# Kernel optimization log

Hardware: AMD Instinct MI355X
Metric: run time of the kernel (lower is better)

The kernel has to match this reference:

```python
import jax, jax.numpy as jnp
import numpy as np

# --- sizes / simulation constants (match init_kwargs) ---
IN_F, OUT_F, BIAS = 512, 512, 1
BATCH = 128
RES, SIM_TIME, TAU_SYN = 1e-4, 2e-2, 5e-3
STEPS = int(np.ceil(SIM_TIME / RES))                 # 200
DECAY_SYN = float(np.exp(-RES / TAU_SYN))
DECAY_MEM = float(np.exp(-RES / TAU_SYN))            # original code uses tau_syn for both


def setup_inputs() -> dict:
    key = jax.random.key(0)
    k1, k2, k3, k4 = jax.random.split(key, 4)
    # input spikes inside the first half of the sim window
    input_times = jax.random.uniform(k1, (BATCH, IN_F), jnp.float32) * (0.5 * SIM_TIME)
    # weights_init = (0.05, 0.1) normal
    weights = 0.05 + 0.1 * jax.random.normal(k2, (IN_F + BIAS, OUT_F), jnp.float32)
    # delays_init = (0.001, 0.0005) normal, kept non-negative
    delays = jnp.abs(0.001 + 0.0005 * jax.random.normal(k3, (IN_F + BIAS, OUT_F), jnp.float32))
    # thresholds_init = (1.0, 0.05) normal
    thresholds = 1.0 + 0.05 * jax.random.normal(k4, (OUT_F,), jnp.float32)
    return {"input_times": input_times, "weights": weights,
            "delays": delays, "thresholds": thresholds}


def _snn_forward(input_times, weights, delays, thresholds):
    B = input_times.shape[0]
    dt = input_times.dtype
    # bias inputs spike at t = 0
    times = jnp.concatenate([input_times, jnp.zeros((B, BIAS), dt)], axis=1)   # [B, I+bias]
    # per-synapse delayed arrival times -> time-step indices
    arrival = times[:, :, None] + delays[None]                                  # [B, I+bias, O]
    step_idx = jnp.clip(jnp.round(arrival / RES).astype(jnp.int32), 0, STEPS - 1)
    b_idx = jnp.arange(B)[:, None, None]
    o_idx = jnp.arange(OUT_F)[None, None, :]
    w = jnp.broadcast_to(weights[None], arrival.shape)
    # charge[b, t, o] = sum_i w[i,o] * 1[arrival step of synapse (i,o) == t]
    charge = jnp.zeros((B, STEPS, OUT_F), dt).at[b_idx, step_idx, o_idx].add(w)
    charge = jnp.moveaxis(charge, 1, 0)                                         # [steps, B, O]

    thr = thresholds[None]                                                      # [1, O]

    def body(carry, inp):
        syn, mem, spike_t, spiked = carry
        t, c = inp
        syn_n = syn * DECAY_SYN + c
        mem_n = mem * DECAY_MEM + (1.0 - DECAY_MEM) * syn_n
        crossing = jnp.logical_and(~spiked, mem_n >= thr)
        denom = mem_n - mem
        safe = jnp.where(jnp.abs(denom) > 1e-12, denom, 1e-12)
        frac = jnp.clip((thr - mem) / safe, 0.0, 1.0)     # linear interp inside the step
        t_cross = (t + frac) * RES
        spike_t = jnp.where(crossing, t_cross, spike_t)
        spiked = jnp.logical_or(spiked, crossing)
        return (syn_n, mem_n, spike_t, spiked), None

    init = (jnp.zeros((B, OUT_F), dt),
            jnp.zeros((B, OUT_F), dt),
            jnp.full((B, OUT_F), SIM_TIME, dt),           # "no spike" -> sim_time
            jnp.zeros((B, OUT_F), bool))
    ts = jnp.arange(STEPS, dtype=dt)
    (syn, mem, spike_t, spiked), _ = jax.lax.scan(body, init, (ts, charge))
    return spike_t                                        # [B, O] first-spike times


def reference(input_times, weights, delays, thresholds):
    return _snn_forward(input_times, weights, delays, thresholds)
```

## Files before the change

### kernel.cpp

```cpp
#include <hip/hip_runtime.h>


#define IN_F    512
#define OUT_F   512
#define BATCH   128
#define STEPS   200
#define RES_F   1e-4f
#define CSTRIDE 33
#define DECAY_F 0.98019867330675525f
#define ONEMD_F 0.019801326693244747f
#define SIM_T_F 2e-2f
#define FPSCALE 8388608.0f
#define INVSCALE 1.1920928955078125e-07f

__device__ __forceinline__ int bin_of(float arr) {
    float q = (float)((double)arr * 10000.0);
    int s = __float2int_rn(q);
    return s > STEPS - 1 ? STEPS - 1 : s;
}

__global__ __launch_bounds__(512, 4) void snn_fwd(
    const float* __restrict__ input_times,
    const float* __restrict__ weights,
    const float* __restrict__ delays,
    const float* __restrict__ thresholds,
    float* __restrict__ out)
{
#pragma clang fp contract(off)
    __shared__ __align__(16) int chargeI[2][STEPS * CSTRIDE];
    __shared__ float times_s[2][IN_F];

    const int tid  = threadIdx.x;
    const int wv   = tid >> 6;
    const int lane = tid & 63;
    const int b0    = (blockIdx.x >> 4) << 1;
    const int otile = blockIdx.x & 15;
    const int ob    = otile << 5;

    {
        int4 z = make_int4(0, 0, 0, 0);
        int4* c4 = (int4*)&chargeI[0][0];
        for (int k = tid; k < (2 * STEPS * CSTRIDE) / 4; k += 512) c4[k] = z;
    }
    times_s[0][tid] = input_times[b0 * IN_F + tid];
    times_s[1][tid] = input_times[(b0 + 1) * IN_F + tid];
    __syncthreads();

    const int sub = lane >> 3;
    const int cgi = lane & 7;
    const int cg  = cgi << 2;
    const float4* __restrict__ Wp = (const float4*)weights;
    const float4* __restrict__ Dp = (const float4*)delays;
    const int r0   = wv << 6;
    const int i0   = (r0 + sub) * (OUT_F / 4) + (ob >> 2) + cgi;
    const int gstr = 8 * (OUT_F / 4);

    if (wv == 7) {
        const int bt = lane >> 5, col = lane & 31;
        float dl = delays[IN_F * OUT_F + ob + col];
        int   wt = __float2int_rn(weights[IN_F * OUT_F + ob + col] * FPSCALE);
        atomicAdd(&chargeI[bt][bin_of(dl) * CSTRIDE + col], wt);
    }

    float4 wA = Wp[i0],            wB = Wp[i0 + gstr];
    float4 dA = Dp[i0],            dB = Dp[i0 + gstr];
    float  tA0 = times_s[0][r0 + sub],     tA1 = times_s[1][r0 + sub];
    float  tB0 = times_s[0][r0 + 8 + sub], tB1 = times_s[1][r0 + 8 + sub];

    #pragma unroll
    for (int g = 0; g < 8; g += 2) {
        float4 wC = {}, wD = {};
        float4 dC = {}, dD = {};
        float  tC0 = 0.f, tC1 = 0.f, tD0 = 0.f, tD1 = 0.f;
        if (g + 2 < 8) {
            wC = Wp[i0 + (g + 2) * gstr]; dC = Dp[i0 + (g + 2) * gstr];
            tC0 = times_s[0][r0 + ((g + 2) << 3) + sub];
            tC1 = times_s[1][r0 + ((g + 2) << 3) + sub];
        }
        if (g + 3 < 8) {
            wD = Wp[i0 + (g + 3) * gstr]; dD = Dp[i0 + (g + 3) * gstr];
            tD0 = times_s[0][r0 + ((g + 3) << 3) + sub];
            tD1 = times_s[1][r0 + ((g + 3) << 3) + sub];
        }
        {
            const float* dv = (const float*)&dA;
            const float* wf = (const float*)&wA;
            #pragma unroll
            for (int k = 0; k < 4; ++k) {
                int wt = __float2int_rn(wf[k] * FPSCALE);
                atomicAdd(&chargeI[0][bin_of(tA0 + dv[k]) * CSTRIDE + cg + k], wt);
                atomicAdd(&chargeI[1][bin_of(tA1 + dv[k]) * CSTRIDE + cg + k], wt);
            }
        }
        {
            const float* dv = (const float*)&dB;
            const float* wf = (const float*)&wB;
            #pragma unroll
            for (int k = 0; k < 4; ++k) {
                int wt = __float2int_rn(wf[k] * FPSCALE);
                atomicAdd(&chargeI[0][bin_of(tB0 + dv[k]) * CSTRIDE + cg + k], wt);
                atomicAdd(&chargeI[1][bin_of(tB1 + dv[k]) * CSTRIDE + cg + k], wt);
            }
        }
        wA = wC; dA = dC; tA0 = tC0; tA1 = tC1;
        wB = wD; dB = dD; tB0 = tD0; tB1 = tD1;
    }
    __syncthreads();

    if (wv == 0) {
        const int bt = lane >> 5, col = lane & 31;
        const float thr = thresholds[ob + col];
        float syn = 0.f, mem = 0.f, spike_t = SIM_T_F;
        bool spiked = false;
        for (int t0 = 0; t0 < STEPS; t0 += 4) {
            float c[4];
            #pragma unroll
            for (int j = 0; j < 4; ++j)
                c[j] = (float)chargeI[bt][(t0 + j) * CSTRIDE + col] * INVSCALE;
            #pragma unroll
            for (int j = 0; j < 4; ++j) {
                float syn_n = syn * DECAY_F + c[j];
                float mem_n = mem * DECAY_F + ONEMD_F * syn_n;
                if (!spiked && mem_n >= thr) {
                    float denom = mem_n - mem;
                    float safe  = fabsf(denom) > 1e-12f ? denom : 1e-12f;
                    float frac  = (thr - mem) / safe;
                    frac = frac < 0.f ? 0.f : (frac > 1.f ? 1.f : frac);
                    spike_t = ((float)(t0 + j) + frac) * RES_F;
                    spiked  = true;
                }
                syn = syn_n; mem = mem_n;
            }
            if (__all(spiked)) break;
        }
        out[(b0 + bt) * OUT_F + ob + col] = spike_t;
    }
}

extern "C" void kernel_launch(void* const* d_in, const int* in_sizes, int n_in,
                              void* d_out, int out_size, void* d_ws, size_t ws_size,
                              hipStream_t stream) {
    const float* input_times = (const float*)d_in[0];
    const float* weights     = (const float*)d_in[1];
    const float* delays      = (const float*)d_in[2];
    const float* thresholds  = (const float*)d_in[3];
    float* out = (float*)d_out;
    (void)d_ws; (void)ws_size;

    dim3 grid((BATCH / 2) * (OUT_F / 32));
    snn_fwd<<<grid, 512, 0, stream>>>(input_times, weights, delays,
                                      thresholds, out);
}
```

Before: 76.26 us.

## Halve output-column tile per block to double grid size and occupancy

After: 75.26 us. Within noise of the previous version (-1.3%).

```diff
diff --git a/kernel.cpp b/kernel.cpp
--- a/kernel.cpp
+++ b/kernel.cpp
@@ -6,7 +6,8 @@
 #define BATCH   128
 #define STEPS   200
 #define RES_F   1e-4f
-#define CSTRIDE 33
+#define COLS    16
+#define CSTRIDE 17
 #define DECAY_F 0.98019867330675525f
 #define ONEMD_F 0.019801326693244747f
 #define SIM_T_F 2e-2f
@@ -19,7 +20,7 @@
     return s > STEPS - 1 ? STEPS - 1 : s;
 }
 
-__global__ __launch_bounds__(512, 4) void snn_fwd(
+__global__ __launch_bounds__(512, 8) void snn_fwd(
     const float* __restrict__ input_times,
     const float* __restrict__ weights,
     const float* __restrict__ delays,
@@ -33,9 +34,9 @@
     const int tid  = threadIdx.x;
     const int wv   = tid >> 6;
     const int lane = tid & 63;
-    const int b0    = (blockIdx.x >> 4) << 1;
-    const int otile = blockIdx.x & 15;
-    const int ob    = otile << 5;
+    const int b0    = (blockIdx.x >> 5) << 1;
+    const int otile = blockIdx.x & 31;
+    const int ob    = otile << 4;
 
     {
         int4 z = make_int4(0, 0, 0, 0);
@@ -46,41 +47,33 @@
     times_s[1][tid] = input_times[(b0 + 1) * IN_F + tid];
     __syncthreads();
 
-    const int sub = lane >> 3;
-    const int cgi = lane & 7;
+    const int sub = lane >> 2;
+    const int cgi = lane & 3;
     const int cg  = cgi << 2;
     const float4* __restrict__ Wp = (const float4*)weights;
     const float4* __restrict__ Dp = (const float4*)delays;
     const int r0   = wv << 6;
     const int i0   = (r0 + sub) * (OUT_F / 4) + (ob >> 2) + cgi;
-    const int gstr = 8 * (OUT_F / 4);
+    const int gstr = 16 * (OUT_F / 4);
 
-    if (wv == 7) {
-        const int bt = lane >> 5, col = lane & 31;
+    if (wv == 7 && lane < 32) {
+        const int bt = lane >> 4, col = lane & 15;
         float dl = delays[IN_F * OUT_F + ob + col];
         int   wt = __float2int_rn(weights[IN_F * OUT_F + ob + col] * FPSCALE);
         atomicAdd(&chargeI[bt][bin_of(dl) * CSTRIDE + col], wt);
     }
 
-    float4 wA = Wp[i0],            wB = Wp[i0 + gstr];
-    float4 dA = Dp[i0],            dB = Dp[i0 + gstr];
-    float  tA0 = times_s[0][r0 + sub],     tA1 = times_s[1][r0 + sub];
-    float  tB0 = times_s[0][r0 + 8 + sub], tB1 = times_s[1][r0 + 8 + sub];
+    float4 wA = Wp[i0], dA = Dp[i0];
+    float  tA0 = times_s[0][r0 + sub], tA1 = times_s[1][r0 + sub];
 
     #pragma unroll
-    for (int g = 0; g < 8; g += 2) {
-        float4 wC = {}, wD = {};
-        float4 dC = {}, dD = {};
-        float  tC0 = 0.f, tC1 = 0.f, tD0 = 0.f, tD1 = 0.f;
-        if (g + 2 < 8) {
-            wC = Wp[i0 + (g + 2) * gstr]; dC = Dp[i0 + (g + 2) * gstr];
-            tC0 = times_s[0][r0 + ((g + 2) << 3) + sub];
-            tC1 = times_s[1][r0 + ((g + 2) << 3) + sub];
-        }
-        if (g + 3 < 8) {
-            wD = Wp[i0 + (g + 3) * gstr]; dD = Dp[i0 + (g + 3) * gstr];
-            tD0 = times_s[0][r0 + ((g + 3) << 3) + sub];
-            tD1 = times_s[1][r0 + ((g + 3) << 3) + sub];
+    for (int g = 0; g < 4; ++g) {
+        float4 wB = {}, dB = {};
+        float  tB0 = 0.f, tB1 = 0.f;
+        if (g + 1 < 4) {
+            wB = Wp[i0 + (g + 1) * gstr]; dB = Dp[i0 + (g + 1) * gstr];
+            tB0 = times_s[0][r0 + ((g + 1) << 4) + sub];
+            tB1 = times_s[1][r0 + ((g + 1) << 4) + sub];
         }
         {
             const float* dv = (const float*)&dA;
@@ -92,23 +85,13 @@
                 atomicAdd(&chargeI[1][bin_of(tA1 + dv[k]) * CSTRIDE + cg + k], wt);
             }
         }
-        {
-            const float* dv = (const float*)&dB;
-            const float* wf = (const float*)&wB;
-            #pragma unroll
-            for (int k = 0; k < 4; ++k) {
-                int wt = __float2int_rn(wf[k] * FPSCALE);
-                atomicAdd(&chargeI[0][bin_of(tB0 + dv[k]) * CSTRIDE + cg + k], wt);
-                atomicAdd(&chargeI[1][bin_of(tB1 + dv[k]) * CSTRIDE + cg + k], wt);
-            }
-        }
-        wA = wC; dA = dC; tA0 = tC0; tA1 = tC1;
-        wB = wD; dB = dD; tB0 = tD0; tB1 = tD1;
+        wA = wB; dA = dB; tA0 = tB0; tA1 = tB1;
     }
     __syncthreads();
 
     if (wv == 0) {
-        const int bt = lane >> 5, col = lane & 31;
+        const int bt  = (lane >> 4) & 1;
+        const int col = lane & 15;
         const float thr = thresholds[ob + col];
         float syn = 0.f, mem = 0.f, spike_t = SIM_T_F;
         bool spiked = false;
@@ -133,7 +116,8 @@
             }
             if (__all(spiked)) break;
         }
-        out[(b0 + bt) * OUT_F + ob + col] = spike_t;
+        if (lane < 32)
+            out[(b0 + bt) * OUT_F + ob + col] = spike_t;
     }
 }
 
@@ -147,7 +131,7 @@
     float* out = (float*)d_out;
     (void)d_ws; (void)ws_size;
 
-    dim3 grid((BATCH / 2) * (OUT_F / 32));
+    dim3 grid((BATCH / 2) * (OUT_F / COLS));
     snn_fwd<<<grid, 512, 0, stream>>>(input_times, weights, delays,
                                       thresholds, out);
 }
```
